# Kernel tuning notes

Measured on AMD Instinct MI355X. Metric: run time of the kernel, lower is better.

## Reference

```python
import jax, jax.numpy as jnp
import numpy as np

B, NUM_RX, NUM_CHIRPS, SAMPLES = 16, 4, 64, 256
D_BINS, R_BINS = 64, 256


def _conv3d(x, w, b, pad):
    y = jax.lax.conv_general_dilated(x, w, (1, 1, 1), pad,
                                     dimension_numbers=('NCDHW', 'OIDHW', 'NCDHW'))
    return y + b[None, :, None, None, None]


def _conv2d(x, w, b, pad):
    y = jax.lax.conv_general_dilated(x, w, (1, 1), pad,
                                     dimension_numbers=('NCHW', 'OIHW', 'NCHW'))
    return y + b[None, :, None, None]


def _bn2(x, s, t):
    return x * s[None, :, None, None] + t[None, :, None, None]


def _bn3(x, s, t):
    return x * s[None, :, None, None, None] + t[None, :, None, None, None]


def _upsample_bilinear_ac(x, oh, ow):
    # torch Upsample(mode='bilinear', align_corners=True)
    _, _, h, w = x.shape
    ph = jnp.linspace(0.0, h - 1.0, oh)
    pw = jnp.linspace(0.0, w - 1.0, ow)
    h0 = jnp.clip(jnp.floor(ph).astype(jnp.int32), 0, h - 1)
    h1 = jnp.clip(h0 + 1, 0, h - 1)
    fh = ph - h0
    w0 = jnp.clip(jnp.floor(pw).astype(jnp.int32), 0, w - 1)
    w1 = jnp.clip(w0 + 1, 0, w - 1)
    fw = pw - w0
    x = x[:, :, h0, :] * (1.0 - fh)[None, None, :, None] + x[:, :, h1, :] * fh[None, None, :, None]
    x = x[:, :, :, w0] * (1.0 - fw) + x[:, :, :, w1] * fw
    return x


def setup_inputs() -> dict:
    ks = iter(jax.random.split(jax.random.key(0), 80))

    def nrm(shape, s=0.05):
        return s * jax.random.normal(next(ks), shape, dtype=jnp.float32)

    inp = {'x': jax.random.normal(next(ks), (B, NUM_RX, NUM_CHIRPS, SAMPLES, 2), dtype=jnp.float32)}

    def conv(name, shape):
        inp[name + '_w'] = nrm(shape)
        inp[name + '_b'] = nrm((shape[0],))

    def bn(name, n):  # BatchNorm in inference form folded to scale/shift
        inp[name + '_s'] = 1.0 + nrm((n,), 0.1)
        inp[name + '_t'] = nrm((n,), 0.1)

    conv('tc1', (16, 2, 1, 1, 3)); bn('tc1', 16)
    conv('tc2', (32, 16, 1, 1, 3)); bn('tc2', 32)
    conv('rx', (32, 32, NUM_RX, 1, 1)); bn('rx', 32)
    conv('cc1', (64, 32 * NUM_CHIRPS, 3, 3)); bn('cc1', 64)
    conv('cc2', (64, 64, 3, 3)); bn('cc2', 64)
    conv('rd1', (128, 64, 3, 3)); bn('rd1', 128)
    conv('rd2', (128, 128, 3, 3)); bn('rd2', 128)
    conv('up1', (64, 128, 3, 3)); bn('up1', 64)
    conv('up2', (32, 64, 3, 3)); bn('up2', 32)
    conv('up3', (1, 32, 1, 1))
    inp['wr'] = jax.random.normal(next(ks), (SAMPLES, R_BINS, 2), dtype=jnp.float32)
    inp['wd'] = jax.random.normal(next(ks), (NUM_CHIRPS, D_BINS, 2), dtype=jnp.float32)
    return inp


def reference(x, tc1_w, tc1_b, tc1_s, tc1_t, tc2_w, tc2_b, tc2_s, tc2_t,
              rx_w, rx_b, rx_s, rx_t, cc1_w, cc1_b, cc1_s, cc1_t,
              cc2_w, cc2_b, cc2_s, cc2_t, rd1_w, rd1_b, rd1_s, rd1_t,
              rd2_w, rd2_b, rd2_s, rd2_t, up1_w, up1_b, up1_s, up1_t,
              up2_w, up2_b, up2_s, up2_t, up3_w, up3_b, wr, wd):
    r = jax.nn.relu
    p3 = [(0, 0), (0, 0), (1, 1)]
    p2 = [(1, 1), (1, 1)]
    h = jnp.transpose(x, (0, 4, 1, 2, 3))                      # [B,2,RX,C,S]
    h = r(_bn3(_conv3d(h, tc1_w, tc1_b, p3), tc1_s, tc1_t))
    h = r(_bn3(_conv3d(h, tc2_w, tc2_b, p3), tc2_s, tc2_t))
    h = r(_bn3(_conv3d(h, rx_w, rx_b, [(0, 0)] * 3), rx_s, rx_t))[:, :, 0]  # [B,32,C,S]
    h = h.reshape(h.shape[0], -1, SAMPLES)[:, :, None, :]      # [B,32*C,1,S]
    h = r(_bn2(_conv2d(h, cc1_w, cc1_b, p2), cc1_s, cc1_t))
    h = r(_bn2(_conv2d(h, cc2_w, cc2_b, p2), cc2_s, cc2_t))
    h = r(_bn2(_conv2d(h, rd1_w, rd1_b, p2), rd1_s, rd1_t))
    h = r(_bn2(_conv2d(h, rd2_w, rd2_b, p2), rd2_s, rd2_t))
    h = _upsample_bilinear_ac(h, D_BINS, R_BINS)               # [B,128,D,R]
    h = r(_bn2(_conv2d(h, up1_w, up1_b, p2), up1_s, up1_t))
    h = r(_bn2(_conv2d(h, up2_w, up2_b, p2), up2_s, up2_t))
    h = jax.nn.sigmoid(_conv2d(h, up3_w, up3_b, [(0, 0), (0, 0)]))  # [B,1,D,R]
    # learnable_fft (input is real: x_imag = 0), loops -> two batched matmuls
    xr = h[:, 0]                                               # [B,D,R]
    rr = jnp.einsum('bcs,sr->bcr', xr, wr[:, :, 0])            # range DFT, real
    ri = jnp.einsum('bcs,sr->bcr', xr, wr[:, :, 1])            # range DFT, imag
    rdr = jnp.einsum('bcr,cd->bdr', rr, wd[:, :, 0]) - jnp.einsum('bcr,cd->bdr', ri, wd[:, :, 1])
    rdi = jnp.einsum('bcr,cd->bdr', rr, wd[:, :, 1]) + jnp.einsum('bcr,cd->bdr', ri, wd[:, :, 0])
    mag = jnp.sqrt(rdr * rdr + rdi * rdi) / (NUM_CHIRPS * SAMPLES)
    out = jnp.clip(h + 0.1 * mag[:, None], 0.0, 1.0)
    return jnp.transpose(out, (0, 2, 3, 1))                    # [B,D,R,1]
```

## Files before the change

kernel.cpp:

```cpp
#include <hip/hip_runtime.h>
#include <math.h>

#define OFF_A      0u
#define OFF_P      8388608u
#define OFF_WCC1   10485760u
#define OFF_BCC1   11010048u
#define OFF_WCC2   11010112u
#define OFF_BCC2   11026496u
#define OFF_WRD1   11026560u
#define OFF_BRD1   11059328u
#define OFF_WRD2   11059456u
#define OFF_BRD2   11124992u
#define OFF_WUP1   11125120u
#define OFF_BUP1   11223424u
#define OFF_WUP2   11223488u
#define OFF_BUP2   11346368u
#define OFF_R      0u
#define OFF_U1     524288u
#define OFF_H      1310720u

__device__ __forceinline__ void fma4(float4& a, const float4& x, float w) {
  a.x = fmaf(x.x, w, a.x); a.y = fmaf(x.y, w, a.y);
  a.z = fmaf(x.z, w, a.z); a.w = fmaf(x.w, w, a.w);
}

__global__ __launch_bounds__(256) void k_repack(
    const float* __restrict__ cc1_w, const float* __restrict__ cc1_b, const float* __restrict__ cc1_s, const float* __restrict__ cc1_t,
    const float* __restrict__ cc2_w, const float* __restrict__ cc2_b, const float* __restrict__ cc2_s, const float* __restrict__ cc2_t,
    const float* __restrict__ rd1_w, const float* __restrict__ rd1_b, const float* __restrict__ rd1_s, const float* __restrict__ rd1_t,
    const float* __restrict__ rd2_w, const float* __restrict__ rd2_b, const float* __restrict__ rd2_s, const float* __restrict__ rd2_t,
    const float* __restrict__ up1_w, const float* __restrict__ up1_b, const float* __restrict__ up1_s, const float* __restrict__ up1_t,
    const float* __restrict__ up2_w, const float* __restrict__ up2_b, const float* __restrict__ up2_s, const float* __restrict__ up2_t,
    float* __restrict__ ws)
{
  const int tid = blockIdx.x * blockDim.x + threadIdx.x;
  const int nth = gridDim.x * blockDim.x;

  for (int i = tid; i < 2048*64*4; i += nth) {
    int k = i & 3, oc = (i >> 2) & 63, c2 = i >> 8;
    ws[OFF_WCC1 + i] = (k < 3) ? cc1_w[((oc*2048 + c2)*3 + 1)*3 + k] * cc1_s[oc] : 0.f;
  }
  for (int i = tid; i < 64; i += nth) ws[OFF_BCC1 + i] = cc1_b[i]*cc1_s[i] + cc1_t[i];

  for (int i = tid; i < 64*64*4; i += nth) {
    int k = i & 3, oc = (i >> 2) & 63, ic = i >> 8;
    ws[OFF_WCC2 + i] = (k < 3) ? cc2_w[((oc*64 + ic)*3 + 1)*3 + k] * cc2_s[oc] : 0.f;
  }
  for (int i = tid; i < 64; i += nth) ws[OFF_BCC2 + i] = cc2_b[i]*cc2_s[i] + cc2_t[i];

  for (int i = tid; i < 64*128*4; i += nth) {
    int k = i & 3, oc = (i >> 2) & 127, ic = i >> 9;
    ws[OFF_WRD1 + i] = (k < 3) ? rd1_w[((oc*64 + ic)*3 + 1)*3 + k] * rd1_s[oc] : 0.f;
  }
  for (int i = tid; i < 128; i += nth) ws[OFF_BRD1 + i] = rd1_b[i]*rd1_s[i] + rd1_t[i];

  for (int i = tid; i < 128*128*4; i += nth) {
    int k = i & 3, oc = (i >> 2) & 127, ic = i >> 9;
    ws[OFF_WRD2 + i] = (k < 3) ? rd2_w[((oc*128 + ic)*3 + 1)*3 + k] * rd2_s[oc] : 0.f;
  }
  for (int i = tid; i < 128; i += nth) ws[OFF_BRD2 + i] = rd2_b[i]*rd2_s[i] + rd2_t[i];

  for (int i = tid; i < 3*128*64*4; i += nth) {
    int k = i & 3, oc = (i >> 2) & 63, ic = (i >> 8) & 127, v = i >> 15;
    float val = 0.f;
    if (k < 3) {
      const int m = (v == 0) ? 6 : (v == 1) ? 7 : 3;
      float a = 0.f;
      for (int kh = 0; kh < 3; ++kh)
        if ((m >> kh) & 1) a += up1_w[((oc*128 + ic)*3 + kh)*3 + k];
      val = a * up1_s[oc];
    }
    ws[OFF_WUP1 + i] = val;
  }
  for (int i = tid; i < 64; i += nth) ws[OFF_BUP1 + i] = up1_b[i]*up1_s[i] + up1_t[i];

  for (int i = tid; i < 5*3*64*32*4; i += nth) {
    int k = i & 3, oc = (i >> 2) & 31, ic = (i >> 7) & 63, t = i >> 13;
    int src = t % 3, v = t / 3;
    float val = 0.f;
    if (k < 3) {
      const int MASKS[15] = {2,4,0,  1,6,0,  0,7,0,  0,3,4,  0,1,2};
      const int m = MASKS[v*3 + src];
      float a = 0.f;
      for (int kh = 0; kh < 3; ++kh)
        if ((m >> kh) & 1) a += up2_w[((oc*64 + ic)*3 + kh)*3 + k];
      val = a * up2_s[oc];
    }
    ws[OFF_WUP2 + i] = val;
  }
  for (int i = tid; i < 32; i += nth) ws[OFF_BUP2 + i] = up2_b[i]*up2_s[i] + up2_t[i];
}

__global__ __launch_bounds__(256) void k_front(
    const float* __restrict__ x,
    const float* __restrict__ w1, const float* __restrict__ b1, const float* __restrict__ s1, const float* __restrict__ t1bn,
    const float* __restrict__ w2, const float* __restrict__ b2, const float* __restrict__ s2, const float* __restrict__ t2bn,
    const float* __restrict__ wrx, const float* __restrict__ brx, const float* __restrict__ srx, const float* __restrict__ trx,
    float* __restrict__ A)
{
  __shared__ __align__(16) float t1s[16][256];
  __shared__ __align__(16) float t2s[32][256];
  __shared__ __align__(16) float w1f[16][6];
  __shared__ float b1f[16];
  __shared__ __align__(16) float w2t[16][3][32];
  __shared__ float b2f[32];
  __shared__ __align__(16) float wrxt[4][32][32];
  __shared__ float brxf[32];

  const int tid = threadIdx.x;
  const int b = blockIdx.x >> 6, chirp = blockIdx.x & 63;

  if (tid < 96) (&w1f[0][0])[tid] = w1[tid] * s1[tid/6];
  if (tid < 16) b1f[tid] = b1[tid]*s1[tid] + t1bn[tid];
  for (int i = tid; i < 1536; i += 256) {
    int oc = i / 48, r = i - oc*48, ic = r / 3, k = r - ic*3;
    w2t[ic][k][oc] = w2[i] * s2[oc];
  }
  if (tid < 32) b2f[tid] = b2[tid]*s2[tid] + t2bn[tid];
  for (int i = tid; i < 4096; i += 256) {
    int rxi = i & 3, ic = (i >> 2) & 31, oc = i >> 7;
    wrxt[rxi][ic][oc] = wrx[i] * srx[oc];
  }
  if (tid < 32) brxf[tid] = brx[tid]*srx[tid] + trx[tid];
  __syncthreads();

  const int s  = tid;
  const int sg = tid & 63;
  const int q  = tid >> 6;
  const int s0 = sg * 4;

  float4 acc[8];
  #pragma unroll
  for (int j = 0; j < 8; ++j) acc[j] = make_float4(0.f, 0.f, 0.f, 0.f);

  #pragma unroll 1
  for (int rxi = 0; rxi < 4; ++rxi) {
    {
      const float2* xb2 = (const float2*)(x + ((size_t)(((b*4 + rxi)*64 + chirp)*256) << 1));
      float2 xm = xb2[s];
      float2 xl = xb2[(s == 0) ? 0 : (s - 1)];
      float2 xr = xb2[(s == 255) ? 255 : (s + 1)];
      if (s == 0)   { xl.x = 0.f; xl.y = 0.f; }
      if (s == 255) { xr.x = 0.f; xr.y = 0.f; }
      #pragma unroll 4
      for (int o = 0; o < 16; ++o) {
        float v = b1f[o];
        v = fmaf(xl.x, w1f[o][0], v);
        v = fmaf(xm.x, w1f[o][1], v);
        v = fmaf(xr.x, w1f[o][2], v);
        v = fmaf(xl.y, w1f[o][3], v);
        v = fmaf(xm.y, w1f[o][4], v);
        v = fmaf(xr.y, w1f[o][5], v);
        t1s[o][s] = fmaxf(v, 0.f);
      }
    }
    __syncthreads();

    {
      float4 t2a[8];
      #pragma unroll
      for (int j = 0; j < 8; ++j) {
        float bv = b2f[q*8 + j];
        t2a[j] = make_float4(bv, bv, bv, bv);
      }
      #pragma unroll 4
      for (int ic = 0; ic < 16; ++ic) {
        float4 tm = *(const float4*)&t1s[ic][s0];
        float tl = t1s[ic][(sg == 0) ? 0 : (s0 - 1)];
        float tr = t1s[ic][(sg == 63) ? 255 : (s0 + 4)];
        if (sg == 0)  tl = 0.f;
        if (sg == 63) tr = 0.f;
        float4 win0 = make_float4(tl, tm.x, tm.y, tm.z);
        float4 win2 = make_float4(tm.y, tm.z, tm.w, tr);
        float4 wA0 = *(const float4*)&w2t[ic][0][q*8];
        float4 wA1 = *(const float4*)&w2t[ic][0][q*8 + 4];
        float4 wB0 = *(const float4*)&w2t[ic][1][q*8];
        float4 wB1 = *(const float4*)&w2t[ic][1][q*8 + 4];
        float4 wC0 = *(const float4*)&w2t[ic][2][q*8];
        float4 wC1 = *(const float4*)&w2t[ic][2][q*8 + 4];
        fma4(t2a[0], win0, wA0.x); fma4(t2a[0], tm, wB0.x); fma4(t2a[0], win2, wC0.x);
        fma4(t2a[1], win0, wA0.y); fma4(t2a[1], tm, wB0.y); fma4(t2a[1], win2, wC0.y);
        fma4(t2a[2], win0, wA0.z); fma4(t2a[2], tm, wB0.z); fma4(t2a[2], win2, wC0.z);
        fma4(t2a[3], win0, wA0.w); fma4(t2a[3], tm, wB0.w); fma4(t2a[3], win2, wC0.w);
        fma4(t2a[4], win0, wA1.x); fma4(t2a[4], tm, wB1.x); fma4(t2a[4], win2, wC1.x);
        fma4(t2a[5], win0, wA1.y); fma4(t2a[5], tm, wB1.y); fma4(t2a[5], win2, wC1.y);
        fma4(t2a[6], win0, wA1.z); fma4(t2a[6], tm, wB1.z); fma4(t2a[6], win2, wC1.z);
        fma4(t2a[7], win0, wA1.w); fma4(t2a[7], tm, wB1.w); fma4(t2a[7], win2, wC1.w);
      }
      #pragma unroll
      for (int j = 0; j < 8; ++j) {
        float4 r;
        r.x = fmaxf(t2a[j].x, 0.f); r.y = fmaxf(t2a[j].y, 0.f);
        r.z = fmaxf(t2a[j].z, 0.f); r.w = fmaxf(t2a[j].w, 0.f);
        *(float4*)&t2s[q*8 + j][s0] = r;
      }
    }
    __syncthreads();

    {
      #pragma unroll 8
      for (int ic = 0; ic < 32; ++ic) {
        float4 tv = *(const float4*)&t2s[ic][s0];
        float4 wa = *(const float4*)&wrxt[rxi][ic][q*8];
        float4 wb = *(const float4*)&wrxt[rxi][ic][q*8 + 4];
        fma4(acc[0], tv, wa.x); fma4(acc[1], tv, wa.y);
        fma4(acc[2], tv, wa.z); fma4(acc[3], tv, wa.w);
        fma4(acc[4], tv, wb.x); fma4(acc[5], tv, wb.y);
        fma4(acc[6], tv, wb.z); fma4(acc[7], tv, wb.w);
      }
    }
    __syncthreads();
  }

  #pragma unroll
  for (int j = 0; j < 8; ++j) {
    int oc = q*8 + j;
    float bb = brxf[oc];
    float4 r;
    r.x = fmaxf(acc[j].x + bb, 0.f); r.y = fmaxf(acc[j].y + bb, 0.f);
    r.z = fmaxf(acc[j].z + bb, 0.f); r.w = fmaxf(acc[j].w + bb, 0.f);
    *(float4*)&A[(size_t)((b*2048 + oc*64 + chirp)*256) + s0] = r;
  }
}

__global__ __launch_bounds__(256) void k_cc1(
    const float* __restrict__ A, const float* __restrict__ wp, float* __restrict__ P)
{
  __shared__ __align__(16) float As[256][36];
  const int tid = threadIdx.x;
  const int ks = blockIdx.x & 7;
  const int stile = (blockIdx.x >> 3) & 7;
  const int b = blockIdx.x >> 6;
  const int s0 = stile * 32;
  const int oc = tid & 63;
  const int sg = tid >> 6;
  const int cbase = ks * 256;
  const float4* w4 = (const float4*)wp;

  for (int i = tid; i < 256*36; i += 256) {
    int c = i / 36, si = i - c*36;
    int sA = s0 - 1 + si;
    float v = 0.f;
    if (si < 34 && sA >= 0 && sA < 256)
      v = A[(size_t)(b*2048 + cbase + c)*256 + sA];
    As[c][si] = v;
  }
  __syncthreads();

  const int sb = sg * 8;
  float4 acc0 = make_float4(0.f,0.f,0.f,0.f);
  float4 acc1 = make_float4(0.f,0.f,0.f,0.f);
  #pragma unroll 4
  for (int c = 0; c < 256; ++c) {
    float4 w = w4[(size_t)(cbase + c)*64 + oc];
    float4 a0 = *(const float4*)&As[c][sb];
    float4 a1 = *(const float4*)&As[c][sb + 4];
    float2 a2 = *(const float2*)&As[c][sb + 8];
    acc0.x = fmaf(a0.x,w.x, fmaf(a0.y,w.y, fmaf(a0.z,w.z, acc0.x)));
    acc0.y = fmaf(a0.y,w.x, fmaf(a0.z,w.y, fmaf(a0.w,w.z, acc0.y)));
    acc0.z = fmaf(a0.z,w.x, fmaf(a0.w,w.y, fmaf(a1.x,w.z, acc0.z)));
    acc0.w = fmaf(a0.w,w.x, fmaf(a1.x,w.y, fmaf(a1.y,w.z, acc0.w)));
    acc1.x = fmaf(a1.x,w.x, fmaf(a1.y,w.y, fmaf(a1.z,w.z, acc1.x)));
    acc1.y = fmaf(a1.y,w.x, fmaf(a1.z,w.y, fmaf(a1.w,w.z, acc1.y)));
    acc1.z = fmaf(a1.z,w.x, fmaf(a1.w,w.y, fmaf(a2.x,w.z, acc1.z)));
    acc1.w = fmaf(a1.w,w.x, fmaf(a2.x,w.y, fmaf(a2.y,w.z, acc1.w)));
  }
  float* Pk = P + ((size_t)(ks*16 + b)*256)*64;
  int s = s0 + sb;
  Pk[(size_t)(s+0)*64 + oc] = acc0.x;
  Pk[(size_t)(s+1)*64 + oc] = acc0.y;
  Pk[(size_t)(s+2)*64 + oc] = acc0.z;
  Pk[(size_t)(s+3)*64 + oc] = acc0.w;
  Pk[(size_t)(s+4)*64 + oc] = acc1.x;
  Pk[(size_t)(s+5)*64 + oc] = acc1.y;
  Pk[(size_t)(s+6)*64 + oc] = acc1.z;
  Pk[(size_t)(s+7)*64 + oc] = acc1.w;
}

__global__ __launch_bounds__(256) void k_mid(
    const float* __restrict__ P, const float* __restrict__ bcc1,
    const float* __restrict__ wcc2, const float* __restrict__ bcc2,
    const float* __restrict__ wrd1, const float* __restrict__ brd1,
    const float* __restrict__ wrd2, const float* __restrict__ brd2,
    float* __restrict__ R)
{
  __shared__ float c1s[14][64];
  __shared__ float c2s[14][64];
  __shared__ float r1s[10][128];
  const int tid = threadIdx.x;
  const int b = blockIdx.x >> 5;
  const int s0 = (blockIdx.x & 31) * 8;
  const float4* wc2 = (const float4*)wcc2;
  const float4* wr1 = (const float4*)wrd1;
  const float4* wr2 = (const float4*)wrd2;

  for (int i = tid; i < 14*64; i += 256) {
    int si = i >> 6, ic = i & 63;
    int sA = s0 - 3 + si;
    float v = 0.f;
    if (sA >= 0 && sA < 256) {
      float a = bcc1[ic];
      #pragma unroll
      for (int ksp = 0; ksp < 8; ++ksp)
        a += P[((size_t)(ksp*16 + b)*256 + sA)*64 + ic];
      v = fmaxf(a, 0.f);
    }
    c1s[si][ic] = v;
  }
  __syncthreads();

  {
    const int g = tid >> 6, oc = tid & 63;
    if (g < 3) {
      float4 acc;
      float bb = bcc2[oc];
      acc = make_float4(bb, bb, bb, bb);
      for (int ic = 0; ic < 64; ++ic) {
        float4 w = wc2[ic*64 + oc];
        float c0 = c1s[g*4+0][ic], c1 = c1s[g*4+1][ic], c2 = c1s[g*4+2][ic];
        float c3 = c1s[g*4+3][ic], c4 = c1s[g*4+4][ic], c5 = c1s[g*4+5][ic];
        acc.x = fmaf(c0,w.x, fmaf(c1,w.y, fmaf(c2,w.z, acc.x)));
        acc.y = fmaf(c1,w.x, fmaf(c2,w.y, fmaf(c3,w.z, acc.y)));
        acc.z = fmaf(c2,w.x, fmaf(c3,w.y, fmaf(c4,w.z, acc.z)));
        acc.w = fmaf(c3,w.x, fmaf(c4,w.y, fmaf(c5,w.z, acc.w)));
      }
      c2s[g*4+0][oc] = fmaxf(acc.x, 0.f);
      c2s[g*4+1][oc] = fmaxf(acc.y, 0.f);
      c2s[g*4+2][oc] = fmaxf(acc.z, 0.f);
      c2s[g*4+3][oc] = fmaxf(acc.w, 0.f);
    } else {
      int k = tid - 192;
      c2s[12][k] = 0.f;
      c2s[13][k] = 0.f;
    }
  }
  __syncthreads();

  for (int it = tid; it < 384; it += 256) {
    const int oc = it & 127, g = it >> 7;
    float4 acc;
    float bb = brd1[oc];
    acc = make_float4(bb, bb, bb, bb);
    for (int ic = 0; ic < 64; ++ic) {
      float4 w = wr1[ic*128 + oc];
      float c0 = c2s[g*4+0][ic], c1 = c2s[g*4+1][ic], c2 = c2s[g*4+2][ic];
      float c3 = c2s[g*4+3][ic], c4 = c2s[g*4+4][ic], c5 = c2s[g*4+5][ic];
      acc.x = fmaf(c0,w.x, fmaf(c1,w.y, fmaf(c2,w.z, acc.x)));
      acc.y = fmaf(c1,w.x, fmaf(c2,w.y, fmaf(c3,w.z, acc.y)));
      acc.z = fmaf(c2,w.x, fmaf(c3,w.y, fmaf(c4,w.z, acc.z)));
      acc.w = fmaf(c3,w.x, fmaf(c4,w.y, fmaf(c5,w.z, acc.w)));
    }
    r1s[g*4+0][oc] = fmaxf(acc.x, 0.f);
    r1s[g*4+1][oc] = fmaxf(acc.y, 0.f);
    if (g < 2) {
      r1s[g*4+2][oc] = fmaxf(acc.z, 0.f);
      r1s[g*4+3][oc] = fmaxf(acc.w, 0.f);
    }
  }
  __syncthreads();

  {
    const int g = tid >> 7, oc = tid & 127;
    float4 acc;
    float bb = brd2[oc];
    acc = make_float4(bb, bb, bb, bb);
    for (int ic = 0; ic < 128; ++ic) {
      float4 w = wr2[ic*128 + oc];
      float c0 = r1s[g*4+0][ic], c1 = r1s[g*4+1][ic], c2 = r1s[g*4+2][ic];
      float c3 = r1s[g*4+3][ic], c4 = r1s[g*4+4][ic], c5 = r1s[g*4+5][ic];
      acc.x = fmaf(c0,w.x, fmaf(c1,w.y, fmaf(c2,w.z, acc.x)));
      acc.y = fmaf(c1,w.x, fmaf(c2,w.y, fmaf(c3,w.z, acc.y)));
      acc.z = fmaf(c2,w.x, fmaf(c3,w.y, fmaf(c4,w.z, acc.z)));
      acc.w = fmaf(c3,w.x, fmaf(c4,w.y, fmaf(c5,w.z, acc.w)));
    }
    int s = s0 + g*4;
    R[((size_t)b*256 + s+0)*128 + oc] = fmaxf(acc.x, 0.f);
    R[((size_t)b*256 + s+1)*128 + oc] = fmaxf(acc.y, 0.f);
    R[((size_t)b*256 + s+2)*128 + oc] = fmaxf(acc.z, 0.f);
    R[((size_t)b*256 + s+3)*128 + oc] = fmaxf(acc.w, 0.f);
  }
}

__global__ __launch_bounds__(192) void k_up1(
    const float* __restrict__ R, const float* __restrict__ wup1, const float* __restrict__ bup1,
    float* __restrict__ U1)
{
  __shared__ float Rs[10][128];
  const int tid = threadIdx.x;
  const int b = blockIdx.x >> 5;
  const int s0 = (blockIdx.x & 31) * 8;
  for (int i = tid; i < 10*128; i += 192) {
    int si = i >> 7, ic = i & 127;
    int sA = s0 - 1 + si;
    Rs[si][ic] = (sA >= 0 && sA < 256) ? R[((size_t)b*256 + sA)*128 + ic] : 0.f;
  }
  __syncthreads();
  const int vi = tid >> 6, oc = tid & 63;
  const float4* w4 = (const float4*)wup1;
  float acc[8];
  float bb = bup1[oc];
  #pragma unroll
  for (int j = 0; j < 8; ++j) acc[j] = bb;
  for (int ic = 0; ic < 128; ++ic) {
    float4 w = w4[(vi*128 + ic)*64 + oc];
    float r0 = Rs[0][ic], r1 = Rs[1][ic], r2 = Rs[2][ic], r3 = Rs[3][ic], r4 = Rs[4][ic];
    float r5 = Rs[5][ic], r6 = Rs[6][ic], r7 = Rs[7][ic], r8 = Rs[8][ic], r9 = Rs[9][ic];
    acc[0] = fmaf(r0,w.x, fmaf(r1,w.y, fmaf(r2,w.z, acc[0])));
    acc[1] = fmaf(r1,w.x, fmaf(r2,w.y, fmaf(r3,w.z, acc[1])));
    acc[2] = fmaf(r2,w.x, fmaf(r3,w.y, fmaf(r4,w.z, acc[2])));
    acc[3] = fmaf(r3,w.x, fmaf(r4,w.y, fmaf(r5,w.z, acc[3])));
    acc[4] = fmaf(r4,w.x, fmaf(r5,w.y, fmaf(r6,w.z, acc[4])));
    acc[5] = fmaf(r5,w.x, fmaf(r6,w.y, fmaf(r7,w.z, acc[5])));
    acc[6] = fmaf(r6,w.x, fmaf(r7,w.y, fmaf(r8,w.z, acc[6])));
    acc[7] = fmaf(r7,w.x, fmaf(r8,w.y, fmaf(r9,w.z, acc[7])));
  }
  #pragma unroll
  for (int j = 0; j < 8; ++j)
    U1[((size_t)(b*3 + vi)*256 + s0 + j)*64 + oc] = fmaxf(acc[j], 0.f);
}

__global__ __launch_bounds__(192) void k_up2(
    const float* __restrict__ U1, const float* __restrict__ wup2, const float* __restrict__ bup2,
    const float* __restrict__ up3_w, const float* __restrict__ up3_b,
    float* __restrict__ H)
{
  __shared__ float u1s[3][10][64];
  __shared__ float u2s[5][32][9];
  const int tid = threadIdx.x;
  const int b = blockIdx.x >> 5;
  const int s0 = (blockIdx.x & 31) * 8;
  for (int i = tid; i < 3*10*64; i += 192) {
    int v = i / 640, r = i - v*640, si = r >> 6, ic = r & 63;
    int sA = s0 - 1 + si;
    u1s[v][si][ic] = (sA >= 0 && sA < 256) ? U1[((size_t)(b*3 + v)*256 + sA)*64 + ic] : 0.f;
  }
  __syncthreads();
  if (tid < 160) {
    const int v = tid >> 5, oc = tid & 31;
    const float4* w4 = (const float4*)wup2;
    float acc[8];
    float bb = bup2[oc];
    #pragma unroll
    for (int j = 0; j < 8; ++j) acc[j] = bb;
    for (int src = 0; src < 3; ++src)
      for (int ic = 0; ic < 64; ++ic) {
        float4 w = w4[((v*3 + src)*64 + ic)*32 + oc];
        float r0 = u1s[src][0][ic], r1 = u1s[src][1][ic], r2 = u1s[src][2][ic];
        float r3 = u1s[src][3][ic], r4 = u1s[src][4][ic], r5 = u1s[src][5][ic];
        float r6 = u1s[src][6][ic], r7 = u1s[src][7][ic], r8 = u1s[src][8][ic];
        float r9 = u1s[src][9][ic];
        acc[0] = fmaf(r0,w.x, fmaf(r1,w.y, fmaf(r2,w.z, acc[0])));
        acc[1] = fmaf(r1,w.x, fmaf(r2,w.y, fmaf(r3,w.z, acc[1])));
        acc[2] = fmaf(r2,w.x, fmaf(r3,w.y, fmaf(r4,w.z, acc[2])));
        acc[3] = fmaf(r3,w.x, fmaf(r4,w.y, fmaf(r5,w.z, acc[3])));
        acc[4] = fmaf(r4,w.x, fmaf(r5,w.y, fmaf(r6,w.z, acc[4])));
        acc[5] = fmaf(r5,w.x, fmaf(r6,w.y, fmaf(r7,w.z, acc[5])));
        acc[6] = fmaf(r6,w.x, fmaf(r7,w.y, fmaf(r8,w.z, acc[6])));
        acc[7] = fmaf(r7,w.x, fmaf(r8,w.y, fmaf(r9,w.z, acc[7])));
      }
    #pragma unroll
    for (int j = 0; j < 8; ++j) u2s[v][oc][j] = fmaxf(acc[j], 0.f);
  }
  __syncthreads();
  if (tid < 40) {
    int v = tid >> 3, j = tid & 7;
    float a = up3_b[0];
    for (int ic = 0; ic < 32; ++ic)
      a = fmaf(u2s[v][ic][j], up3_w[ic], a);
    H[(size_t)(b*5 + v)*256 + s0 + j] = 1.f / (1.f + expf(-a));
  }
}

__global__ __launch_bounds__(64) void k_spec(
    const float* __restrict__ H, const float* __restrict__ wr, const float* __restrict__ wd,
    float* __restrict__ out)
{
  __shared__ float hs[5][256];
  __shared__ float S0[64], S1[64];
  __shared__ float wds[4][64][2];
  const int tid = threadIdx.x;
  const int b = blockIdx.x >> 2;
  const int rt = blockIdx.x & 3;
  for (int i = tid; i < 1280; i += 64) hs[i >> 8][i & 255] = H[(size_t)b*1280 + i];
  {
    float a0 = 0.f, a1 = 0.f;
    for (int c = 2; c <= 61; ++c) {
      a0 += wd[(c*64 + tid)*2 + 0];
      a1 += wd[(c*64 + tid)*2 + 1];
    }
    S0[tid] = a0; S1[tid] = a1;
  }
  for (int i = tid; i < 512; i += 64) {
    int row = i >> 7, rem = i & 127, d = rem >> 1, comp = rem & 1;
    int c = (row < 2) ? row : (60 + row);
    wds[row][d][comp] = wd[(c*64 + d)*2 + comp];
  }
  __syncthreads();
  const int r = rt*64 + tid;
  float rr0=0,rr1=0,rr2=0,rr3=0,rr4=0, ri0=0,ri1=0,ri2=0,ri3=0,ri4=0;
  const float2* wr2p = (const float2*)wr;
  for (int s = 0; s < 256; ++s) {
    float2 w = wr2p[s*256 + r];
    float h0 = hs[0][s], h1 = hs[1][s], h2 = hs[2][s], h3 = hs[3][s], h4 = hs[4][s];
    rr0 = fmaf(h0, w.x, rr0); ri0 = fmaf(h0, w.y, ri0);
    rr1 = fmaf(h1, w.x, rr1); ri1 = fmaf(h1, w.y, ri1);
    rr2 = fmaf(h2, w.x, rr2); ri2 = fmaf(h2, w.y, ri2);
    rr3 = fmaf(h3, w.x, rr3); ri3 = fmaf(h3, w.y, ri3);
    rr4 = fmaf(h4, w.x, rr4); ri4 = fmaf(h4, w.y, ri4);
  }
  for (int d = 0; d < 64; ++d) {
    float w0r = wds[0][d][0], w0i = wds[0][d][1];
    float w1r = wds[1][d][0], w1i = wds[1][d][1];
    float w2r = wds[2][d][0], w2i = wds[2][d][1];
    float w3r = wds[3][d][0], w3i = wds[3][d][1];
    float s0v = S0[d], s1v = S1[d];
    float rdr = rr0*w0r + rr1*w1r + rr2*s0v + rr3*w2r + rr4*w3r
              - ri0*w0i - ri1*w1i - ri2*s1v - ri3*w2i - ri4*w3i;
    float rdi = rr0*w0i + rr1*w1i + rr2*s1v + rr3*w2i + rr4*w3i
              + ri0*w0r + ri1*w1r + ri2*s0v + ri3*w2r + ri4*w3r;
    float mag = sqrtf(rdr*rdr + rdi*rdi) * (1.0f / 16384.0f);
    int v = (d == 0) ? 0 : (d == 1) ? 1 : (d <= 61) ? 2 : ((d == 62) ? 3 : 4);
    float o = hs[v][r] + 0.1f * mag;
    out[(size_t)b*16384 + d*256 + r] = fminf(fmaxf(o, 0.f), 1.f);
  }
}

extern "C" void kernel_launch(void* const* d_in, const int* in_sizes, int n_in,
                              void* d_out, int out_size, void* d_ws, size_t ws_size,
                              hipStream_t stream)
{
  const float* x     = (const float*)d_in[0];
  const float* tc1_w = (const float*)d_in[1];  const float* tc1_b = (const float*)d_in[2];
  const float* tc1_s = (const float*)d_in[3];  const float* tc1_t = (const float*)d_in[4];
  const float* tc2_w = (const float*)d_in[5];  const float* tc2_b = (const float*)d_in[6];
  const float* tc2_s = (const float*)d_in[7];  const float* tc2_t = (const float*)d_in[8];
  const float* rx_w  = (const float*)d_in[9];  const float* rx_b  = (const float*)d_in[10];
  const float* rx_s  = (const float*)d_in[11]; const float* rx_t  = (const float*)d_in[12];
  const float* cc1_w = (const float*)d_in[13]; const float* cc1_b = (const float*)d_in[14];
  const float* cc1_s = (const float*)d_in[15]; const float* cc1_t = (const float*)d_in[16];
  const float* cc2_w = (const float*)d_in[17]; const float* cc2_b = (const float*)d_in[18];
  const float* cc2_s = (const float*)d_in[19]; const float* cc2_t = (const float*)d_in[20];
  const float* rd1_w = (const float*)d_in[21]; const float* rd1_b = (const float*)d_in[22];
  const float* rd1_s = (const float*)d_in[23]; const float* rd1_t = (const float*)d_in[24];
  const float* rd2_w = (const float*)d_in[25]; const float* rd2_b = (const float*)d_in[26];
  const float* rd2_s = (const float*)d_in[27]; const float* rd2_t = (const float*)d_in[28];
  const float* up1_w = (const float*)d_in[29]; const float* up1_b = (const float*)d_in[30];
  const float* up1_s = (const float*)d_in[31]; const float* up1_t = (const float*)d_in[32];
  const float* up2_w = (const float*)d_in[33]; const float* up2_b = (const float*)d_in[34];
  const float* up2_s = (const float*)d_in[35]; const float* up2_t = (const float*)d_in[36];
  const float* up3_w = (const float*)d_in[37]; const float* up3_b = (const float*)d_in[38];
  const float* wr    = (const float*)d_in[39];
  const float* wd    = (const float*)d_in[40];
  float* ws  = (float*)d_ws;
  float* out = (float*)d_out;

  k_repack<<<1024, 256, 0, stream>>>(cc1_w, cc1_b, cc1_s, cc1_t,
                                     cc2_w, cc2_b, cc2_s, cc2_t,
                                     rd1_w, rd1_b, rd1_s, rd1_t,
                                     rd2_w, rd2_b, rd2_s, rd2_t,
                                     up1_w, up1_b, up1_s, up1_t,
                                     up2_w, up2_b, up2_s, up2_t, ws);
  k_front<<<1024, 256, 0, stream>>>(x, tc1_w, tc1_b, tc1_s, tc1_t,
                                    tc2_w, tc2_b, tc2_s, tc2_t,
                                    rx_w, rx_b, rx_s, rx_t, ws + OFF_A);
  k_cc1<<<1024, 256, 0, stream>>>(ws + OFF_A, ws + OFF_WCC1, ws + OFF_P);
  k_mid<<<512, 256, 0, stream>>>(ws + OFF_P, ws + OFF_BCC1,
                                 ws + OFF_WCC2, ws + OFF_BCC2,
                                 ws + OFF_WRD1, ws + OFF_BRD1,
                                 ws + OFF_WRD2, ws + OFF_BRD2, ws + OFF_R);
  k_up1<<<512, 192, 0, stream>>>(ws + OFF_R, ws + OFF_WUP1, ws + OFF_BUP1, ws + OFF_U1);
  k_up2<<<512, 192, 0, stream>>>(ws + OFF_U1, ws + OFF_WUP2, ws + OFF_BUP2, up3_w, up3_b, ws + OFF_H);
  k_spec<<<64, 64, 0, stream>>>(ws + OFF_H, wr, wd, out);
}
```

Baseline: 417.5 us.

## Split front-end channel mixing into halves and read prefolded rx weights from global

The rx conv weights are now prefolded with their BN scale once in the repack kernel and read by k_front straight from global/L2, instead of being rebuilt into a 16 KB shared table by every block. The tc2 stage is split into two 16-channel halves, which halves the t2s shared buffer. Together these cut shared memory per block so more blocks can be resident, and they remove the per-block weight setup. The cost is an extra barrier pair per half and weight loads through the cache in the inner loop.

```diff
diff --git a/kernel.cpp b/kernel.cpp
--- a/kernel.cpp
+++ b/kernel.cpp
@@ -15,6 +15,7 @@
 #define OFF_BUP1   11223424u
 #define OFF_WUP2   11223488u
 #define OFF_BUP2   11346368u
+#define OFF_WRX    11346400u
 #define OFF_R      0u
 #define OFF_U1     524288u
 #define OFF_H      1310720u
@@ -25,6 +26,7 @@
 }
 
 __global__ __launch_bounds__(256) void k_repack(
+    const float* __restrict__ rx_w, const float* __restrict__ rx_s,
     const float* __restrict__ cc1_w, const float* __restrict__ cc1_b, const float* __restrict__ cc1_s, const float* __restrict__ cc1_t,
     const float* __restrict__ cc2_w, const float* __restrict__ cc2_b, const float* __restrict__ cc2_s, const float* __restrict__ cc2_t,
     const float* __restrict__ rd1_w, const float* __restrict__ rd1_b, const float* __restrict__ rd1_s, const float* __restrict__ rd1_t,
@@ -35,6 +37,11 @@
 {
   const int tid = blockIdx.x * blockDim.x + threadIdx.x;
   const int nth = gridDim.x * blockDim.x;
+
+  for (int i = tid; i < 4096; i += nth) {
+    int oc = i & 31, ic = (i >> 5) & 31, rxi = i >> 10;
+    ws[OFF_WRX + i] = rx_w[(oc*32 + ic)*4 + rxi] * rx_s[oc];
+  }
 
   for (int i = tid; i < 2048*64*4; i += nth) {
     int k = i & 3, oc = (i >> 2) & 63, c2 = i >> 8;
@@ -95,16 +102,15 @@
     const float* __restrict__ x,
     const float* __restrict__ w1, const float* __restrict__ b1, const float* __restrict__ s1, const float* __restrict__ t1bn,
     const float* __restrict__ w2, const float* __restrict__ b2, const float* __restrict__ s2, const float* __restrict__ t2bn,
-    const float* __restrict__ wrx, const float* __restrict__ brx, const float* __restrict__ srx, const float* __restrict__ trx,
+    const float* __restrict__ wrxF, const float* __restrict__ brx, const float* __restrict__ srx, const float* __restrict__ trx,
     float* __restrict__ A)
 {
   __shared__ __align__(16) float t1s[16][256];
-  __shared__ __align__(16) float t2s[32][256];
+  __shared__ __align__(16) float t2s[16][256];
   __shared__ __align__(16) float w1f[16][6];
   __shared__ float b1f[16];
   __shared__ __align__(16) float w2t[16][3][32];
   __shared__ float b2f[32];
-  __shared__ __align__(16) float wrxt[4][32][32];
   __shared__ float brxf[32];
 
   const int tid = threadIdx.x;
@@ -117,10 +123,6 @@
     w2t[ic][k][oc] = w2[i] * s2[oc];
   }
   if (tid < 32) b2f[tid] = b2[tid]*s2[tid] + t2bn[tid];
-  for (int i = tid; i < 4096; i += 256) {
-    int rxi = i & 3, ic = (i >> 2) & 31, oc = i >> 7;
-    wrxt[rxi][ic][oc] = wrx[i] * srx[oc];
-  }
   if (tid < 32) brxf[tid] = brx[tid]*srx[tid] + trx[tid];
   __syncthreads();
 
@@ -156,60 +158,58 @@
     }
     __syncthreads();
 
-    {
-      float4 t2a[8];
-      #pragma unroll
-      for (int j = 0; j < 8; ++j) {
-        float bv = b2f[q*8 + j];
-        t2a[j] = make_float4(bv, bv, bv, bv);
+    #pragma unroll 1
+    for (int h = 0; h < 2; ++h) {
+      {
+        const int ocb = h*16 + q*4;
+        float4 t2a[4];
+        #pragma unroll
+        for (int j = 0; j < 4; ++j) {
+          float bv = b2f[ocb + j];
+          t2a[j] = make_float4(bv, bv, bv, bv);
+        }
+        #pragma unroll 4
+        for (int ic = 0; ic < 16; ++ic) {
+          float4 tm = *(const float4*)&t1s[ic][s0];
+          float tl = t1s[ic][(sg == 0) ? 0 : (s0 - 1)];
+          float tr = t1s[ic][(sg == 63) ? 255 : (s0 + 4)];
+          if (sg == 0)  tl = 0.f;
+          if (sg == 63) tr = 0.f;
+          float4 win0 = make_float4(tl, tm.x, tm.y, tm.z);
+          float4 win2 = make_float4(tm.y, tm.z, tm.w, tr);
+          float4 wA = *(const float4*)&w2t[ic][0][ocb];
+          float4 wB = *(const float4*)&w2t[ic][1][ocb];
+          float4 wC = *(const float4*)&w2t[ic][2][ocb];
+          fma4(t2a[0], win0, wA.x); fma4(t2a[0], tm, wB.x); fma4(t2a[0], win2, wC.x);
+          fma4(t2a[1], win0, wA.y); fma4(t2a[1], tm, wB.y); fma4(t2a[1], win2, wC.y);
+          fma4(t2a[2], win0, wA.z); fma4(t2a[2], tm, wB.z); fma4(t2a[2], win2, wC.z);
+          fma4(t2a[3], win0, wA.w); fma4(t2a[3], tm, wB.w); fma4(t2a[3], win2, wC.w);
+        }
+        #pragma unroll
+        for (int j = 0; j < 4; ++j) {
+          float4 r;
+          r.x = fmaxf(t2a[j].x, 0.f); r.y = fmaxf(t2a[j].y, 0.f);
+          r.z = fmaxf(t2a[j].z, 0.f); r.w = fmaxf(t2a[j].w, 0.f);
+          *(float4*)&t2s[q*4 + j][s0] = r;
+        }
       }
-      #pragma unroll 4
-      for (int ic = 0; ic < 16; ++ic) {
-        float4 tm = *(const float4*)&t1s[ic][s0];
-        float tl = t1s[ic][(sg == 0) ? 0 : (s0 - 1)];
-        float tr = t1s[ic][(sg == 63) ? 255 : (s0 + 4)];
-        if (sg == 0)  tl = 0.f;
-        if (sg == 63) tr = 0.f;
-        float4 win0 = make_float4(tl, tm.x, tm.y, tm.z);
-        float4 win2 = make_float4(tm.y, tm.z, tm.w, tr);
-        float4 wA0 = *(const float4*)&w2t[ic][0][q*8];
-        float4 wA1 = *(const float4*)&w2t[ic][0][q*8 + 4];
-        float4 wB0 = *(const float4*)&w2t[ic][1][q*8];
-        float4 wB1 = *(const float4*)&w2t[ic][1][q*8 + 4];
-        float4 wC0 = *(const float4*)&w2t[ic][2][q*8];
-        float4 wC1 = *(const float4*)&w2t[ic][2][q*8 + 4];
-        fma4(t2a[0], win0, wA0.x); fma4(t2a[0], tm, wB0.x); fma4(t2a[0], win2, wC0.x);
-        fma4(t2a[1], win0, wA0.y); fma4(t2a[1], tm, wB0.y); fma4(t2a[1], win2, wC0.y);
-        fma4(t2a[2], win0, wA0.z); fma4(t2a[2], tm, wB0.z); fma4(t2a[2], win2, wC0.z);
-        fma4(t2a[3], win0, wA0.w); fma4(t2a[3], tm, wB0.w); fma4(t2a[3], win2, wC0.w);
-        fma4(t2a[4], win0, wA1.x); fma4(t2a[4], tm, wB1.x); fma4(t2a[4], win2, wC1.x);
-        fma4(t2a[5], win0, wA1.y); fma4(t2a[5], tm, wB1.y); fma4(t2a[5], win2, wC1.y);
-        fma4(t2a[6], win0, wA1.z); fma4(t2a[6], tm, wB1.z); fma4(t2a[6], win2, wC1.z);
-        fma4(t2a[7], win0, wA1.w); fma4(t2a[7], tm, wB1.w); fma4(t2a[7], win2, wC1.w);
+      __syncthreads();
+
+      {
+        const float* wbase = wrxF + ((rxi*32 + h*16)*32) + q*8;
+        #pragma unroll 8
+        for (int ic = 0; ic < 16; ++ic) {
+          float4 tv = *(const float4*)&t2s[ic][s0];
+          float4 wa = *(const float4*)(wbase + ic*32);
+          float4 wb = *(const float4*)(wbase + ic*32 + 4);
+          fma4(acc[0], tv, wa.x); fma4(acc[1], tv, wa.y);
+          fma4(acc[2], tv, wa.z); fma4(acc[3], tv, wa.w);
+          fma4(acc[4], tv, wb.x); fma4(acc[5], tv, wb.y);
+          fma4(acc[6], tv, wb.z); fma4(acc[7], tv, wb.w);
+        }
       }
-      #pragma unroll
-      for (int j = 0; j < 8; ++j) {
-        float4 r;
-        r.x = fmaxf(t2a[j].x, 0.f); r.y = fmaxf(t2a[j].y, 0.f);
-        r.z = fmaxf(t2a[j].z, 0.f); r.w = fmaxf(t2a[j].w, 0.f);
-        *(float4*)&t2s[q*8 + j][s0] = r;
-      }
-    }
-    __syncthreads();
-
-    {
-      #pragma unroll 8
-      for (int ic = 0; ic < 32; ++ic) {
-        float4 tv = *(const float4*)&t2s[ic][s0];
-        float4 wa = *(const float4*)&wrxt[rxi][ic][q*8];
-        float4 wb = *(const float4*)&wrxt[rxi][ic][q*8 + 4];
-        fma4(acc[0], tv, wa.x); fma4(acc[1], tv, wa.y);
-        fma4(acc[2], tv, wa.z); fma4(acc[3], tv, wa.w);
-        fma4(acc[4], tv, wb.x); fma4(acc[5], tv, wb.y);
-        fma4(acc[6], tv, wb.z); fma4(acc[7], tv, wb.w);
-      }
-    }
-    __syncthreads();
+      __syncthreads();
+    }
   }
 
   #pragma unroll
@@ -554,7 +554,8 @@
   float* ws  = (float*)d_ws;
   float* out = (float*)d_out;
 
-  k_repack<<<1024, 256, 0, stream>>>(cc1_w, cc1_b, cc1_s, cc1_t,
+  k_repack<<<1024, 256, 0, stream>>>(rx_w, rx_s,
+                                     cc1_w, cc1_b, cc1_s, cc1_t,
                                      cc2_w, cc2_b, cc2_s, cc2_t,
                                      rd1_w, rd1_b, rd1_s, rd1_t,
                                      rd2_w, rd2_b, rd2_s, rd2_t,
@@ -562,7 +563,7 @@
                                      up2_w, up2_b, up2_s, up2_t, ws);
   k_front<<<1024, 256, 0, stream>>>(x, tc1_w, tc1_b, tc1_s, tc1_t,
                                     tc2_w, tc2_b, tc2_s, tc2_t,
-                                    rx_w, rx_b, rx_s, rx_t, ws + OFF_A);
+                                    ws + OFF_WRX, rx_b, rx_s, rx_t, ws + OFF_A);
   k_cc1<<<1024, 256, 0, stream>>>(ws + OFF_A, ws + OFF_WCC1, ws + OFF_P);
   k_mid<<<512, 256, 0, stream>>>(ws + OFF_P, ws + OFF_BCC1,
                                  ws + OFF_WCC2, ws + OFF_BCC2,
```

Measured after the change: 420.4 us. No clear change (+0.7%).
